# Optimization experiments

Measured on AMD Instinct MI355X. Metric: run time of the kernel, lower is better.

Reference implementation:

```python
import jax, jax.numpy as jnp
import numpy as np

NUM_HEADS = 16


def setup_inputs() -> dict:
    key = jax.random.key(0)
    ks = jax.random.split(key, 6)
    B, S, H = 4, 2048, 1024
    x = jax.random.normal(ks[0], (B, S, H), dtype=jnp.float32)
    mask = jax.random.randint(ks[1], (B, 1, 1, S), 0, 2, dtype=jnp.int32)
    scale = 1.0 / np.sqrt(H)
    Wq = jax.random.normal(ks[2], (H, H), dtype=jnp.float32) * scale
    Wk = jax.random.normal(ks[3], (H, H), dtype=jnp.float32) * scale
    Wv = jax.random.normal(ks[4], (H, H), dtype=jnp.float32) * scale
    Wo = jax.random.normal(ks[5], (H, H), dtype=jnp.float32) * scale
    bo = jnp.zeros((H,), dtype=jnp.float32)
    return {"x": x, "mask": mask, "Wq": Wq, "Wk": Wk, "Wv": Wv, "Wo": Wo, "bo": bo}


def reference(x, mask, Wq, Wk, Wv, Wo, bo):
    B, S, H = x.shape
    nh = NUM_HEADS
    dk = H // nh

    def split_heads(t):  # (B,S,H) -> (B,nh,S,dk)
        return t.reshape(B, S, nh, dk).transpose(0, 2, 1, 3)

    # torch Linear: y = x @ W.T (q/k/v bias-free)
    q = split_heads(x @ Wq.T)
    k = split_heads(x @ Wk.T)
    v = split_heads(x @ Wv.T)

    scores = jnp.einsum('bhqd,bhkd->bhqk', q, k) / jnp.sqrt(jnp.float32(dk))
    scores = jnp.where(mask == 0, jnp.float32(-1e9), scores)
    attn = jax.nn.softmax(scores, axis=-1)  # dropout is identity in eval mode
    out = jnp.einsum('bhqk,bhkd->bhqd', attn, v)
    out = out.transpose(0, 2, 1, 3).reshape(B, S, H)
    return out @ Wo.T + bo
```

## Files before the change

kernel.cpp:

```cpp
#include <hip/hip_runtime.h>
#include <hip/hip_bf16.h>

typedef __attribute__((ext_vector_type(8))) short sh8;
typedef __attribute__((ext_vector_type(4))) float f32x4;

#define MFMA16(a, b, c) __builtin_amdgcn_mfma_f32_16x16x32_bf16((a), (b), (c), 0, 0, 0)

__device__ __forceinline__ unsigned short f2bf(float f) {
    return (unsigned short)((__float_as_uint(f) + 0x8000u) >> 16);
}
__device__ __forceinline__ unsigned int pack2bf(float lo, float hi) {
    unsigned int ul = __float_as_uint(lo) + 0x8000u;
    unsigned int uh = __float_as_uint(hi) + 0x8000u;
    return __builtin_amdgcn_perm(uh, ul, 0x07060302u);
}
__device__ __forceinline__ float redmax_hi(float x) {
    x = fmaxf(x, __shfl_xor(x, 16, 64));
    return fmaxf(x, __shfl_xor(x, 32, 64));
}
__device__ __forceinline__ float redsum_hi(float x) {
    x += __shfl_xor(x, 16, 64);
    return x + __shfl_xor(x, 32, 64);
}
__device__ __forceinline__ void gload_lds16(const void* g, void* l) {
    __builtin_amdgcn_global_load_lds(
        (const __attribute__((address_space(1))) unsigned int*)g,
        (__attribute__((address_space(3))) unsigned int*)l, 16, 0, 0);
}

__global__ __launch_bounds__(256) void cvt_x_k(
    const float* __restrict__ src, unsigned short* __restrict__ dst, int n4)
{
    int i = blockIdx.x * 256 + threadIdx.x;
    int stride = gridDim.x * 256;
    for (; i < n4; i += stride) {
        float4 v = ((const float4*)src)[i];
        uint2 h = { pack2bf(v.x, v.y), pack2bf(v.z, v.w) };
        ((uint2*)dst)[i] = h;
    }
}
__global__ __launch_bounds__(256) void cvt_w_k(
    const float* __restrict__ Wq, const float* __restrict__ Wk,
    const float* __restrict__ Wv, const float* __restrict__ Wo,
    unsigned short* __restrict__ wbf)
{
    int i = blockIdx.x * 256 + threadIdx.x;
    int seg = i >> 18;
    int off = i & 0x3FFFF;
    const float* s = (seg < 2) ? ((seg == 0) ? Wq : Wk) : ((seg == 2) ? Wv : Wo);
    float4 v = ((const float4*)s)[off];
    uint2 h = { pack2bf(v.x, v.y), pack2bf(v.z, v.w) };
    ((uint2*)wbf)[i] = h;
}

__global__ __launch_bounds__(64) void compact_k(
    const int* __restrict__ mask, int* __restrict__ idx, int* __restrict__ cnt)
{
    const int b = blockIdx.x, l = threadIdx.x;
    const int* mb = mask + b * 2048;
    int base = 0;
    for (int i = 0; i < 32; ++i) {
        int m = mb[i * 64 + l];
        unsigned long long bal = __ballot(m != 0);
        int pre = __popcll(bal & ((1ull << l) - 1ull));
        if (m) idx[b * 2048 + base + pre] = i * 64 + l;
        base += (int)__popcll(bal);
    }
    if (base == 0) {
        for (int i = l; i < 2048; i += 64) idx[b * 2048 + i] = i;
        base = 2048;
    }
    if (l == 0) cnt[b] = base;
}

__global__ __launch_bounds__(256) void kvgather_k(
    const unsigned short* __restrict__ qkv, const int* __restrict__ idx,
    const int* __restrict__ cnt, unsigned short* __restrict__ Kc, int b0)
{
    const int b = blockIdx.z;
    const int t = blockIdx.y;
    const int z = blockIdx.x;
    const int nc = cnt[b0 + b];
    if (t * 64 >= ((nc + 63) & ~63)) return;
    const int* idxb = idx + (size_t)(b0 + b) * 2048;
    const int tid = threadIdx.x;
    unsigned short* dst_b = Kc + (size_t)b * 2048 * 2048;
#pragma unroll
    for (int p = 0; p < 8; ++p) {
        int row = t * 64 + z * 8 + p;
        int src = idxb[min(row, nc - 1)];
        uint4 v = *(const uint4*)&qkv[((size_t)b * 2048 + src) * 3072 + 1024 + tid * 8];
        *(uint4*)&dst_b[(size_t)row * 2048 + tid * 8] = v;
    }
}

__global__ __launch_bounds__(256) void gemm_qkv_k(
    const unsigned short* __restrict__ xbf,
    const unsigned short* __restrict__ wbf,
    unsigned short* __restrict__ qkv)
{
    __shared__ unsigned short As[128][32];
    __shared__ unsigned short Bs[128][32];
    const int tid = threadIdx.x;
    const int l = tid & 63, w = tid >> 6;
    const int wr = w >> 1, wc = w & 1;
    const long row0 = (long)blockIdx.y * 128;
    const int col0 = blockIdx.x * 128;

    f32x4 acc[4][4] = {};
    const int fr = l & 15, hi = l >> 4;

    const int sr = tid >> 2;
    const int sc = (tid & 3) * 8;
    const unsigned short* ga = &xbf[(row0 + sr) * 1024 + sc];
    const unsigned short* gb = &wbf[(long)(col0 + sr) * 1024 + sc];
    unsigned short* la = &As[w * 16][0];
    unsigned short* lb = &Bs[w * 16][0];

    for (int k0 = 0; k0 < 1024; k0 += 32) {
        __syncthreads();
        gload_lds16(ga + k0, la);
        gload_lds16(ga + 64 * 1024 + k0, la + 64 * 32);
        gload_lds16(gb + k0, lb);
        gload_lds16(gb + 64 * 1024 + k0, lb + 64 * 32);
        __syncthreads();

        sh8 af[4], bf[4];
#pragma unroll
        for (int i = 0; i < 4; ++i) {
            af[i] = *(const sh8*)&As[wr * 64 + i * 16 + fr][hi * 8];
            bf[i] = *(const sh8*)&Bs[wc * 64 + i * 16 + fr][hi * 8];
        }
#pragma unroll
        for (int i = 0; i < 4; ++i)
#pragma unroll
            for (int j = 0; j < 4; ++j)
                acc[i][j] = MFMA16(af[i], bf[j], acc[i][j]);
    }

    const float scale = (col0 < 1024) ? 0.1803368801f : 1.0f;
    const int rg = hi * 4, cg = l & 15;
#pragma unroll
    for (int i = 0; i < 4; ++i)
#pragma unroll
        for (int j = 0; j < 4; ++j) {
            long gr = row0 + wr * 64 + i * 16 + rg;
            int gc = col0 + wc * 64 + j * 16 + cg;
#pragma unroll
            for (int r = 0; r < 4; ++r)
                qkv[(gr + r) * 3072 + gc] = f2bf(acc[i][j][r] * scale);
        }
}

__global__ __launch_bounds__(256) void attn_k(
    const unsigned short* __restrict__ qkv, const unsigned short* __restrict__ Kc,
    const int* __restrict__ cnt, unsigned short* __restrict__ ao, int b0)
{
    __shared__ unsigned short Kl[64][64];
    __shared__ unsigned short Vt[64][64];
    __shared__ float biasf[64];
    __shared__ unsigned short Pl[4][16][72];

    const int tid = threadIdx.x;
    const int l = tid & 63, w = tid >> 6;
    const int fr = l & 15, hi = l >> 4;

    int nwg = gridDim.x;
    int wgid = ((nwg & 7) == 0) ? ((blockIdx.x & 7) * (nwg >> 3) + (blockIdx.x >> 3))
                                : blockIdx.x;
    const int qb = wgid & 31;
    const int h  = (wgid >> 5) & 15;
    const int b  = wgid >> 9;
    const int q0 = qb * 64;
    const long base = (long)b * 2048;

    const int nc = cnt[b0 + b];
    const int nt = (nc + 63) >> 6;

    sh8 qf0, qf1;
    {
        const unsigned short* qp = &qkv[(base + q0 + w * 16 + fr) * 3072 + h * 64 + hi * 8];
        qf0 = *(const sh8*)qp;
        qf1 = *(const sh8*)(qp + 32);
    }

    f32x4 acc[4] = {};
    float mrow = -1e30f;
    float lrow = 0.f;

    const long TS = 262144;
    const char* kc_b = (const char*)Kc + (size_t)b * 2048 * 4096;

    const int l8 = l >> 3, c8 = l & 7;
    const char* ksrc = kc_b + (size_t)(w * 16 + l8) * 4096 + h * 128 + ((c8 ^ l8) * 16);
    unsigned short* kdst0 = &Kl[w * 16][0];
    unsigned short* kdst1 = &Kl[w * 16 + 8][0];

    const int kv2 = tid >> 3, dc = tid & 7;
    const char* vp0 = kc_b + (size_t)(2 * kv2) * 4096 + 2048 + h * 128 + dc * 16;
    uint4 v0r = *(const uint4*)vp0;
    uint4 v1r = *(const uint4*)(vp0 + 4096);
    vp0 += TS;

    for (int t = 0; t < nt; ++t) {
        __syncthreads();
        gload_lds16(ksrc, kdst0);
        gload_lds16(ksrc + 8 * 4096, kdst1);
        ksrc += TS;
        {
            unsigned int w0[4] = { v0r.x, v0r.y, v0r.z, v0r.w };
            unsigned int w1[4] = { v1r.x, v1r.y, v1r.z, v1r.w };
            int cc2 = kv2 >> 2, pos = (2 * kv2) & 7;
#pragma unroll
            for (int jj = 0; jj < 4; ++jj) {
                int de = dc * 8 + 2 * jj;
                unsigned int pe = (w0[jj] & 0xffffu) | (w1[jj] << 16);
                unsigned int po = (w0[jj] >> 16) | (w1[jj] & 0xffff0000u);
                int fde = (2 * jj) ^ dc;
                int fdo = (2 * jj + 1) ^ dc;
                *(unsigned int*)&Vt[de][((cc2 ^ fde) * 8) + pos] = pe;
                *(unsigned int*)&Vt[de + 1][((cc2 ^ fdo) * 8) + pos] = po;
            }
        }
        if (tid < 64) biasf[tid] = (t * 64 + tid < nc) ? 0.0f : -1e9f;
        __syncthreads();

        if (t + 1 < nt) {
            v0r = *(const uint4*)vp0;
            v1r = *(const uint4*)(vp0 + 4096);
            vp0 += TS;
        }

        sh8 kf[4][2];
#pragma unroll
        for (int tt = 0; tt < 4; ++tt) {
            const unsigned short* kp = &Kl[tt * 16 + fr][0];
#pragma unroll
            for (int c = 0; c < 2; ++c)
                kf[tt][c] = *(const sh8*)&kp[((4 * c + hi) ^ (fr & 7)) * 8];
        }

        f32x4 s[4] = {};
        __builtin_amdgcn_s_setprio(1);
#pragma unroll
        for (int tt = 0; tt < 4; ++tt) {
            s[tt] = MFMA16(kf[tt][0], qf0, s[tt]);
            s[tt] = MFMA16(kf[tt][1], qf1, s[tt]);
        }
        __builtin_amdgcn_s_setprio(0);
#pragma unroll
        for (int tt = 0; tt < 4; ++tt)
            s[tt] += *(const f32x4*)&biasf[tt * 16 + 4 * hi];

        float pm = s[0][0];
#pragma unroll
        for (int tt = 0; tt < 4; ++tt)
#pragma unroll
            for (int r = 0; r < 4; ++r) pm = fmaxf(pm, s[tt][r]);
        pm = redmax_hi(pm);

        if (!__all(pm <= mrow)) {
            float mn = fmaxf(mrow, pm);
            float scl = __builtin_amdgcn_exp2f(mrow - mn);
            lrow *= scl;
#pragma unroll
            for (int df = 0; df < 4; ++df) acc[df] *= scl;
            mrow = mn;
        }

        float ps = 0.f;
#pragma unroll
        for (int tt = 0; tt < 4; ++tt)
#pragma unroll
            for (int r = 0; r < 4; ++r) {
                float p = __builtin_amdgcn_exp2f(s[tt][r] - mrow);
                s[tt][r] = p;
                ps += p;
            }
        lrow += redsum_hi(ps);

#pragma unroll
        for (int tt = 0; tt < 4; ++tt) {
            uint2 pw = { pack2bf(s[tt][0], s[tt][1]), pack2bf(s[tt][2], s[tt][3]) };
            *(uint2*)&Pl[w][fr][tt * 16 + hi * 4] = pw;
        }

#pragma unroll
        for (int c = 0; c < 2; ++c) {
            sh8 pa = *(const sh8*)&Pl[w][fr][c * 32 + hi * 8];
            __builtin_amdgcn_s_setprio(1);
#pragma unroll
            for (int df = 0; df < 4; ++df) {
                int d = df * 16 + fr;
                int fd = (d & 7) ^ (d >> 3);
                sh8 vfr = *(const sh8*)&Vt[d][((4 * c + hi) ^ fd) * 8];
                acc[df] = MFMA16(vfr, pa, acc[df]);
            }
            __builtin_amdgcn_s_setprio(0);
        }
    }

    {
        float inv = 1.0f / lrow;
        long qr = base + q0 + w * 16 + fr;
        unsigned short* op = &ao[qr * 1024 + h * 64];
#pragma unroll
        for (int df = 0; df < 4; ++df) {
            f32x4 o = acc[df];
            uint2 ow = { pack2bf(o[0] * inv, o[1] * inv), pack2bf(o[2] * inv, o[3] * inv) };
            *(uint2*)&op[df * 16 + hi * 4] = ow;
        }
    }
}

__global__ __launch_bounds__(256) void gemm_out_k(
    const unsigned short* __restrict__ ao, const unsigned short* __restrict__ wob,
    const float* __restrict__ bo, float* __restrict__ out)
{
    __shared__ unsigned short As[128][32];
    __shared__ unsigned short Bs[128][32];
    const int tid = threadIdx.x;
    const int l = tid & 63, w = tid >> 6;
    const int wr = w >> 1, wc = w & 1;
    const long row0 = (long)blockIdx.y * 128;
    const int col0 = blockIdx.x * 128;

    f32x4 acc[4][4] = {};
    const int fr = l & 15, hi = l >> 4;

    const int sr = tid >> 2;
    const int sc = (tid & 3) * 8;
    const unsigned short* ga = &ao[(row0 + sr) * 1024 + sc];
    const unsigned short* gb = &wob[(long)(col0 + sr) * 1024 + sc];
    unsigned short* la = &As[w * 16][0];
    unsigned short* lb = &Bs[w * 16][0];

    for (int k0 = 0; k0 < 1024; k0 += 32) {
        __syncthreads();
        gload_lds16(ga + k0, la);
        gload_lds16(ga + 64 * 1024 + k0, la + 64 * 32);
        gload_lds16(gb + k0, lb);
        gload_lds16(gb + 64 * 1024 + k0, lb + 64 * 32);
        __syncthreads();

        sh8 af[4], bf[4];
#pragma unroll
        for (int i = 0; i < 4; ++i) {
            af[i] = *(const sh8*)&As[wr * 64 + i * 16 + fr][hi * 8];
            bf[i] = *(const sh8*)&Bs[wc * 64 + i * 16 + fr][hi * 8];
        }
#pragma unroll
        for (int i = 0; i < 4; ++i)
#pragma unroll
            for (int j = 0; j < 4; ++j)
                acc[i][j] = MFMA16(af[i], bf[j], acc[i][j]);
    }

    const int rg = hi * 4, cg = l & 15;
#pragma unroll
    for (int i = 0; i < 4; ++i)
#pragma unroll
        for (int j = 0; j < 4; ++j) {
            long gr = row0 + wr * 64 + i * 16 + rg;
            int gc = col0 + wc * 64 + j * 16 + cg;
            float bb = bo[gc];
#pragma unroll
            for (int r = 0; r < 4; ++r)
                out[(gr + r) * 1024 + gc] = acc[i][j][r] + bb;
        }
}

extern "C" void kernel_launch(void* const* d_in, const int* in_sizes, int n_in,
                              void* d_out, int out_size, void* d_ws, size_t ws_size,
                              hipStream_t stream) {
    const float* x    = (const float*)d_in[0];
    const int*   mask = (const int*)d_in[1];
    const float* Wq   = (const float*)d_in[2];
    const float* Wk   = (const float*)d_in[3];
    const float* Wv   = (const float*)d_in[4];
    const float* Wo   = (const float*)d_in[5];
    const float* bo   = (const float*)d_in[6];
    float* out = (float*)d_out;

    const size_t wbf_bytes = (size_t)4096 * 1024 * 2;
    const size_t idx_bytes = (size_t)4 * 2048 * 4 + 64;
    const size_t xbf_per_b = (size_t)2048 * 1024 * 2;
    const size_t qkv_per_b = (size_t)2048 * 3072 * 2;
    const size_t ao_per_b  = (size_t)2048 * 1024 * 2;
    const size_t kc_per_b  = (size_t)2048 * 2048 * 2;
    const size_t per_b = xbf_per_b + qkv_per_b + ao_per_b + kc_per_b;

    size_t fixed = wbf_bytes + idx_bytes;
    size_t avail = (ws_size > fixed) ? (ws_size - fixed) : 0;
    int bchunk = (avail >= per_b) ? (int)(avail / per_b) : 1;
    if (bchunk > 4) bchunk = 4;

    char* p = (char*)d_ws;
    unsigned short* wbf = (unsigned short*)p;            p += wbf_bytes;
    int* idxp = (int*)p;                                 p += (size_t)4 * 2048 * 4;
    int* cntp = (int*)p;                                 p += 64;
    unsigned short* xbf = (unsigned short*)p;            p += (size_t)bchunk * xbf_per_b;
    unsigned short* qkv = (unsigned short*)p;            p += (size_t)bchunk * qkv_per_b;
    unsigned short* ao  = (unsigned short*)p;            p += (size_t)bchunk * ao_per_b;
    unsigned short* Kc  = (unsigned short*)p;

    cvt_w_k<<<4096, 256, 0, stream>>>(Wq, Wk, Wv, Wo, wbf);
    compact_k<<<4, 64, 0, stream>>>(mask, idxp, cntp);

    for (int b0 = 0; b0 < 4; b0 += bchunk) {
        int bc = (4 - b0 < bchunk) ? (4 - b0) : bchunk;
        cvt_x_k<<<2048, 256, 0, stream>>>(
            x + (size_t)b0 * 2048 * 1024, xbf, bc * 524288);
        gemm_qkv_k<<<dim3(24, bc * 16), 256, 0, stream>>>(xbf, wbf, qkv);
        kvgather_k<<<dim3(8, 32, bc), 256, 0, stream>>>(qkv, idxp, cntp, Kc, b0);
        attn_k<<<dim3(512 * bc), 256, 0, stream>>>(qkv, Kc, cntp, ao, b0);
        gemm_out_k<<<dim3(8, bc * 16), 256, 0, stream>>>(
            ao, wbf + (size_t)3072 * 1024, bo, out + (size_t)b0 * 2048 * 1024);
    }
}
```

Baseline: 210.0 us.

## Pre-transpose V into global buffer and stream via direct LDS loads

Adds a kernel that transposes the gathered V per head into a d-major global buffer. The attention kernel can then load V tiles straight into LDS with async global-to-LDS copies, using an XOR swizzle, instead of loading into registers, repacking and scattering to LDS on every tile. This takes the transpose work off the attention inner loop. The cost is an extra launch, extra global traffic and more workspace. vtrans_k transposes all 2048 rows regardless of the masked count.

```diff
diff --git a/kernel.cpp b/kernel.cpp
--- a/kernel.cpp
+++ b/kernel.cpp
@@ -94,6 +94,39 @@
     }
 }
 
+__global__ __launch_bounds__(256) void vtrans_k(
+    const unsigned short* __restrict__ Kc, unsigned short* __restrict__ Vtg)
+{
+    __shared__ unsigned short Ls[128][72];
+    const int kb = blockIdx.x;
+    const int h  = blockIdx.y;
+    const int b  = blockIdx.z;
+    const int tid = threadIdx.x;
+    const unsigned short* src = Kc + (size_t)b * 2048 * 2048 + 1024 + h * 64;
+#pragma unroll
+    for (int p = 0; p < 4; ++p) {
+        int i = p * 256 + tid;
+        int r = i >> 3, c = i & 7;
+        uint4 v = *(const uint4*)&src[((size_t)(kb * 128 + r)) * 2048 + c * 8];
+        *(uint4*)&Ls[r][c * 8] = v;
+    }
+    __syncthreads();
+    unsigned short* dst = Vtg + ((size_t)b * 16 + h) * 64 * 2048;
+#pragma unroll
+    for (int p = 0; p < 4; ++p) {
+        int i = p * 256 + tid;
+        int d = i >> 4, kc = i & 15;
+        unsigned int wv[4];
+#pragma unroll
+        for (int j = 0; j < 4; ++j) {
+            unsigned int lo = Ls[kc * 8 + 2 * j][d];
+            unsigned int hv = Ls[kc * 8 + 2 * j + 1][d];
+            wv[j] = lo | (hv << 16);
+        }
+        *(uint4*)&dst[(size_t)d * 2048 + kb * 128 + kc * 8] = *(uint4*)wv;
+    }
+}
+
 __global__ __launch_bounds__(256) void gemm_qkv_k(
     const unsigned short* __restrict__ xbf,
     const unsigned short* __restrict__ wbf,
@@ -154,7 +187,8 @@
 
 __global__ __launch_bounds__(256) void attn_k(
     const unsigned short* __restrict__ qkv, const unsigned short* __restrict__ Kc,
-    const int* __restrict__ cnt, unsigned short* __restrict__ ao, int b0)
+    const unsigned short* __restrict__ Vtg, const int* __restrict__ cnt,
+    unsigned short* __restrict__ ao, int b0)
 {
     __shared__ unsigned short Kl[64][64];
     __shared__ unsigned short Vt[64][64];
@@ -196,40 +230,24 @@
     unsigned short* kdst0 = &Kl[w * 16][0];
     unsigned short* kdst1 = &Kl[w * 16 + 8][0];
 
-    const int kv2 = tid >> 3, dc = tid & 7;
-    const char* vp0 = kc_b + (size_t)(2 * kv2) * 4096 + 2048 + h * 128 + dc * 16;
-    uint4 v0r = *(const uint4*)vp0;
-    uint4 v1r = *(const uint4*)(vp0 + 4096);
-    vp0 += TS;
+    const char* vtg_h = (const char*)Vtg + ((size_t)b * 16 + h) * 64 * 4096;
+    const int d0 = w * 16 + l8, d1 = d0 + 8;
+    const int fd0 = (d0 & 7) ^ (d0 >> 3), fd1 = (d1 & 7) ^ (d1 >> 3);
+    const char* vsrc0 = vtg_h + (size_t)d0 * 4096 + ((c8 ^ fd0) * 16);
+    const char* vsrc1 = vtg_h + (size_t)d1 * 4096 + ((c8 ^ fd1) * 16);
+    unsigned short* vdst0 = &Vt[w * 16][0];
+    unsigned short* vdst1 = &Vt[w * 16 + 8][0];
 
     for (int t = 0; t < nt; ++t) {
         __syncthreads();
         gload_lds16(ksrc, kdst0);
         gload_lds16(ksrc + 8 * 4096, kdst1);
         ksrc += TS;
-        {
-            unsigned int w0[4] = { v0r.x, v0r.y, v0r.z, v0r.w };
-            unsigned int w1[4] = { v1r.x, v1r.y, v1r.z, v1r.w };
-            int cc2 = kv2 >> 2, pos = (2 * kv2) & 7;
-#pragma unroll
-            for (int jj = 0; jj < 4; ++jj) {
-                int de = dc * 8 + 2 * jj;
-                unsigned int pe = (w0[jj] & 0xffffu) | (w1[jj] << 16);
-                unsigned int po = (w0[jj] >> 16) | (w1[jj] & 0xffff0000u);
-                int fde = (2 * jj) ^ dc;
-                int fdo = (2 * jj + 1) ^ dc;
-                *(unsigned int*)&Vt[de][((cc2 ^ fde) * 8) + pos] = pe;
-                *(unsigned int*)&Vt[de + 1][((cc2 ^ fdo) * 8) + pos] = po;
-            }
-        }
+        gload_lds16(vsrc0, vdst0);
+        gload_lds16(vsrc1, vdst1);
+        vsrc0 += 128; vsrc1 += 128;
         if (tid < 64) biasf[tid] = (t * 64 + tid < nc) ? 0.0f : -1e9f;
         __syncthreads();
-
-        if (t + 1 < nt) {
-            v0r = *(const uint4*)vp0;
-            v1r = *(const uint4*)(vp0 + 4096);
-            vp0 += TS;
-        }
 
         sh8 kf[4][2];
 #pragma unroll
@@ -388,7 +406,8 @@
     const size_t qkv_per_b = (size_t)2048 * 3072 * 2;
     const size_t ao_per_b  = (size_t)2048 * 1024 * 2;
     const size_t kc_per_b  = (size_t)2048 * 2048 * 2;
-    const size_t per_b = xbf_per_b + qkv_per_b + ao_per_b + kc_per_b;
+    const size_t vt_per_b  = (size_t)16 * 64 * 2048 * 2;
+    const size_t per_b = xbf_per_b + qkv_per_b + ao_per_b + kc_per_b + vt_per_b;
 
     size_t fixed = wbf_bytes + idx_bytes;
     size_t avail = (ws_size > fixed) ? (ws_size - fixed) : 0;
@@ -402,7 +421,8 @@
     unsigned short* xbf = (unsigned short*)p;            p += (size_t)bchunk * xbf_per_b;
     unsigned short* qkv = (unsigned short*)p;            p += (size_t)bchunk * qkv_per_b;
     unsigned short* ao  = (unsigned short*)p;            p += (size_t)bchunk * ao_per_b;
-    unsigned short* Kc  = (unsigned short*)p;
+    unsigned short* Kc  = (unsigned short*)p;            p += (size_t)bchunk * kc_per_b;
+    unsigned short* Vtg = (unsigned short*)p;
 
     cvt_w_k<<<4096, 256, 0, stream>>>(Wq, Wk, Wv, Wo, wbf);
     compact_k<<<4, 64, 0, stream>>>(mask, idxp, cntp);
@@ -413,7 +433,8 @@
             x + (size_t)b0 * 2048 * 1024, xbf, bc * 524288);
         gemm_qkv_k<<<dim3(24, bc * 16), 256, 0, stream>>>(xbf, wbf, qkv);
         kvgather_k<<<dim3(8, 32, bc), 256, 0, stream>>>(qkv, idxp, cntp, Kc, b0);
-        attn_k<<<dim3(512 * bc), 256, 0, stream>>>(qkv, Kc, cntp, ao, b0);
+        vtrans_k<<<dim3(16, 16, bc), 256, 0, stream>>>(Kc, Vtg);
+        attn_k<<<dim3(512 * bc), 256, 0, stream>>>(qkv, Kc, Vtg, cntp, ao, b0);
         gemm_out_k<<<dim3(8, bc * 16), 256, 0, stream>>>(
             ao, wbf + (size_t)3072 * 1024, bo, out + (size_t)b0 * 2048 * 1024);
     }
```

Result: slower. 218.2 us (+3.9%).
